# Kernel optimization log

Measured on AMD Instinct MI355X. Metric: run time of the kernel, lower is better.

The kernel has to match this reference:

```python
import jax, jax.numpy as jnp
import numpy as np

VOCAB = 67
EMB = 32
BRANCH = 32
OUT = 96
L = 16
B = 131072


def setup_inputs() -> dict:
    key = jax.random.key(0)
    ks = jax.random.split(key, 10)
    x = jax.random.randint(ks[0], (B, L), 0, VOCAB, dtype=jnp.int64)
    embed = jax.random.normal(ks[1], (VOCAB, EMB), dtype=jnp.float32) * 0.1
    w2 = jax.random.normal(ks[2], (BRANCH, EMB, 2), dtype=jnp.float32) * 0.1
    b2 = jnp.zeros((BRANCH,), jnp.float32)
    w3 = jax.random.normal(ks[3], (BRANCH, EMB, 3), dtype=jnp.float32) * 0.1
    b3 = jnp.zeros((BRANCH,), jnp.float32)
    w4 = jax.random.normal(ks[4], (BRANCH, EMB, 4), dtype=jnp.float32) * 0.1
    b4 = jnp.zeros((BRANCH,), jnp.float32)
    pw = jax.random.normal(ks[5], (OUT, 3 * BRANCH), dtype=jnp.float32) * 0.02
    pb = jnp.zeros((OUT,), jnp.float32)
    return {"x": x, "embed": embed, "w2": w2, "b2": b2, "w3": w3,
            "b3": b3, "w4": w4, "b4": b4, "pw": pw, "pb": pb}


def _branch(emb_ncl, w, b):
    # emb_ncl: [B, EMB, L]; w: [BRANCH, EMB, k] -> conv valid, ReLU, max over time
    y = jax.lax.conv_general_dilated(
        emb_ncl, w, window_strides=(1,), padding='VALID',
        dimension_numbers=('NCH', 'OIH', 'NCH'))
    y = jax.nn.relu(y + b[None, :, None])
    return jnp.max(y, axis=2)  # [B, BRANCH]


def reference(x, embed, w2, b2, w3, b3, w4, b4, pw, pb):
    # padding_idx=0: row 0 of the table is zeros
    table = embed.at[0].set(0.0)
    emb = table[x]                      # [B, L, EMB]
    emb = jnp.transpose(emb, (0, 2, 1))  # [B, EMB, L]
    g2 = _branch(emb, w2, b2)
    g3 = _branch(emb, w3, b3)
    g4 = _branch(emb, w4, b4)
    feat = jnp.concatenate([g2, g3, g4], axis=1)  # [B, 96]
    # Linear + ReLU (dropout is identity at eval)
    return jax.nn.relu(feat @ pw.T + pb)
```

## Files before the change

### kernel.cpp

```cpp
#include <hip/hip_runtime.h>
#include <hip/hip_fp16.h>


#define VOCABSZ 67
#define EMBSZ   32
#define NCH     32
#define NFEAT   96
#define SEQL    16
#define BATCH   131072
#define NTAB    9
#define NFP     (NFEAT / 2)
#define TABU    9648
#define PWOFF   9648
#define NPW     4608
#define CNTW    14336
#define NCHUNK  1024
#define ESTR    80
#define LTS     (VOCABSZ * ESTR)
#define LDSB    (NTAB * LTS + 16)

typedef _Float16 v2h __attribute__((ext_vector_type(2)));
typedef _Float16 v8h __attribute__((ext_vector_type(8)));
typedef float    v4f __attribute__((ext_vector_type(4)));

__device__ __forceinline__ unsigned packh2(float a, float b) {
    v2h p; p[0] = (_Float16)a; p[1] = (_Float16)b;
    return __builtin_bit_cast(unsigned, p);
}

__global__ __launch_bounds__(256) void build_tables(
    const float* __restrict__ embed,
    const float* __restrict__ w2, const float* __restrict__ b2,
    const float* __restrict__ w3, const float* __restrict__ b3,
    const float* __restrict__ w4, const float* __restrict__ b4,
    const float* __restrict__ pw,
    unsigned* __restrict__ ws)
{
    int idx = blockIdx.x * 256 + threadIdx.x;
    if (idx == CNTW) ws[idx] = 0u;
    if (idx < TABU) {
        int cp = idx & 15;
        int t  = idx >> 4;
        int j  = t / VOCABSZ;
        int v  = t - j * VOCABSZ;
        const float* w; const float* bias; int k, h;
        if (j < 2)      { w = w2; k = 2; h = j;     bias = (h == 0) ? b2 : nullptr; }
        else if (j < 5) { w = w3; k = 3; h = j - 2; bias = (h == 0) ? b3 : nullptr; }
        else            { w = w4; k = 4; h = j - 5; bias = (h == 0) ? b4 : nullptr; }
        int c0 = 2 * cp;
        float a0 = bias ? bias[c0]     : 0.0f;
        float a1 = bias ? bias[c0 + 1] : 0.0f;
        if (v != 0) {
            #pragma unroll
            for (int e = 0; e < EMBSZ; ++e) {
                float ev = embed[v * EMBSZ + e];
                a0 += ev * w[((c0    ) * EMBSZ + e) * k + h];
                a1 += ev * w[((c0 + 1) * EMBSZ + e) * k + h];
            }
        }
        ws[t * 16 + cp] = packh2(a0, a1);
    } else if (idx < TABU + NPW) {
        int i  = idx - PWOFF;
        int o  = i / NFP;
        int fp = i - o * NFP;
        ws[PWOFF + i] = packh2(pw[o * NFEAT + 2 * fp], pw[o * NFEAT + 2 * fp + 1]);
    }
}

template<int K, int N, int P0, int TB>
__device__ __forceinline__ void lconv(const char* __restrict__ base,
                                      const int (&ap)[16], v8h& m)
{
    v8h s[N];
    #pragma unroll
    for (int u = 0; u < N; ++u)
        s[u] = *reinterpret_cast<const v8h*>(base + TB + ap[P0 + u]);
    #pragma unroll
    for (int h = 1; h < K; ++h) {
        v8h t[N];
        #pragma unroll
        for (int u = 0; u < N; ++u)
            t[u] = *reinterpret_cast<const v8h*>(base + TB + h * LTS + ap[P0 + u + h]);
        #pragma unroll
        for (int u = 0; u < N; ++u) s[u] = s[u] + t[u];
    }
    #pragma unroll
    for (int u = 0; u < N; ++u) m = __builtin_elementwise_max(m, s[u]);
}

__global__ __launch_bounds__(512, 6) void fused_cnn(
    const int*      __restrict__ x,
    unsigned*       __restrict__ ws,
    const float*    __restrict__ pb,
    float*          __restrict__ out)
{
    extern __shared__ __align__(16) char ldsraw[];
    const int tid = threadIdx.x;
    {
        const float4* s4 = reinterpret_cast<const float4*>(ws);
        float4* d4 = reinterpret_cast<float4*>(ldsraw);
        #pragma unroll
        for (int i0 = 0; i0 < 2560; i0 += 512) {
            int i = i0 + tid;
            if (i < 2412) {
                int t = i >> 2, cc = i & 3;
                d4[5 * t + cc] = s4[i];
            }
        }
    }
    volatile int* slot = reinterpret_cast<volatile int*>(ldsraw + NTAB * LTS);
    unsigned* cnt = ws + CNTW;

    const int lane = tid & 63;
    const int wv   = tid >> 6;
    const int ml   = lane & 15;
    const int c    = lane >> 4;
    const int co   = c << 4;
    const char* base = ldsraw;
    const unsigned* __restrict__ pwp = ws + PWOFF + ml * NFP + c * 4;

    for (;;) {
        if (tid == 0) *slot = (int)atomicAdd(cnt, 1u);
        __syncthreads();
        const int chunk = *slot;
        __syncthreads();
        if (chunk >= NCHUNK) break;

        const int rowb = chunk * 128 + wv * 16;
        const int row  = rowb + ml;

        const int4* xp = reinterpret_cast<const int4*>(x + row * SEQL);
        int4 q0 = xp[0], q1 = xp[1], q2 = xp[2], q3 = xp[3];
        int ap[16];
        ap[ 0] = q0.x * ESTR + co; ap[ 1] = q0.y * ESTR + co;
        ap[ 2] = q0.z * ESTR + co; ap[ 3] = q0.w * ESTR + co;
        ap[ 4] = q1.x * ESTR + co; ap[ 5] = q1.y * ESTR + co;
        ap[ 6] = q1.z * ESTR + co; ap[ 7] = q1.w * ESTR + co;
        ap[ 8] = q2.x * ESTR + co; ap[ 9] = q2.y * ESTR + co;
        ap[10] = q2.z * ESTR + co; ap[11] = q2.w * ESTR + co;
        ap[12] = q3.x * ESTR + co; ap[13] = q3.y * ESTR + co;
        ap[14] = q3.z * ESTR + co; ap[15] = q3.w * ESTR + co;

        v8h m2 = {}, m3 = {}, m4 = {};
        lconv<2, 5,  0, 0 * LTS>(base, ap, m2);
        lconv<2, 5,  5, 0 * LTS>(base, ap, m2);
        lconv<2, 5, 10, 0 * LTS>(base, ap, m2);
        lconv<3, 5,  0, 2 * LTS>(base, ap, m3);
        lconv<3, 5,  5, 2 * LTS>(base, ap, m3);
        lconv<3, 4, 10, 2 * LTS>(base, ap, m3);
        lconv<4, 5,  0, 5 * LTS>(base, ap, m4);
        lconv<4, 4,  5, 5 * LTS>(base, ap, m4);
        lconv<4, 4,  9, 5 * LTS>(base, ap, m4);

        #pragma unroll
        for (int u = 0; u < 6; ++u) {
            v4f acc = {0.f, 0.f, 0.f, 0.f};
            v8h w0 = *reinterpret_cast<const v8h*>(pwp + 768 * u);
            v8h w1 = *reinterpret_cast<const v8h*>(pwp + 768 * u + 16);
            v8h w2 = *reinterpret_cast<const v8h*>(pwp + 768 * u + 32);
            acc = __builtin_amdgcn_mfma_f32_16x16x32_f16(m2, w0, acc, 0, 0, 0);
            acc = __builtin_amdgcn_mfma_f32_16x16x32_f16(m3, w1, acc, 0, 0, 0);
            acc = __builtin_amdgcn_mfma_f32_16x16x32_f16(m4, w2, acc, 0, 0, 0);
            float pbl = pb[16 * u + ml];
            #pragma unroll
            for (int r = 0; r < 4; ++r)
                out[(size_t)(rowb + c * 4 + r) * NFEAT + 16 * u + ml] =
                    fmaxf(acc[r] + pbl, 0.f);
        }
    }
}

extern "C" void kernel_launch(void* const* d_in, const int* in_sizes, int n_in,
                              void* d_out, int out_size, void* d_ws, size_t ws_size,
                              hipStream_t stream)
{
    const int*   x     = (const int*)  d_in[0];
    const float* embed = (const float*)d_in[1];
    const float* w2    = (const float*)d_in[2];
    const float* b2    = (const float*)d_in[3];
    const float* w3    = (const float*)d_in[4];
    const float* b3    = (const float*)d_in[5];
    const float* w4    = (const float*)d_in[6];
    const float* b4    = (const float*)d_in[7];
    const float* pw    = (const float*)d_in[8];
    const float* pb    = (const float*)d_in[9];
    float* out = (float*)d_out;
    unsigned* ws = (unsigned*)d_ws;

    build_tables<<<(CNTW + 256) / 256, 256, 0, stream>>>(
        embed, w2, b2, w3, b3, w4, b4, pw, ws);

    (void)hipFuncSetAttribute((const void*)fused_cnn,
                              hipFuncAttributeMaxDynamicSharedMemorySize,
                              LDSB);
    fused_cnn<<<768, 512, LDSB, stream>>>(x, ws, pb, out);
}
```

Before: 49.45 us.

## Replace persistent atomic-scheduled blocks with one-chunk-per-block grid and unpadded LDS tables

Drops the persistent-kernel loop that fetched 128-row chunks through a global atomic counter, and instead launches one block per chunk (1024 blocks), removing the atomic, the two barriers per chunk and the counter reset. The LDS table row stride shrinks from 80 to 64 bytes, so the table copy becomes a straight contiguous copy and addresses are computed with shifts. The smaller LDS footprint allows raising the launch-bounds occupancy hint from 6 to 8. The trade-off is that every block now reloads the full LDS table once per chunk rather than once per persistent block, and the unpadded stride may increase LDS bank conflicts.

```diff
diff --git a/kernel.cpp b/kernel.cpp
--- a/kernel.cpp
+++ b/kernel.cpp
@@ -13,11 +13,9 @@
 #define TABU    9648
 #define PWOFF   9648
 #define NPW     4608
-#define CNTW    14336
-#define NCHUNK  1024
-#define ESTR    80
+#define ESTR    64
 #define LTS     (VOCABSZ * ESTR)
-#define LDSB    (NTAB * LTS + 16)
+#define LDSB    (NTAB * LTS)
 
 typedef _Float16 v2h __attribute__((ext_vector_type(2)));
 typedef _Float16 v8h __attribute__((ext_vector_type(8)));
@@ -37,7 +35,6 @@
     unsigned* __restrict__ ws)
 {
     int idx = blockIdx.x * 256 + threadIdx.x;
-    if (idx == CNTW) ws[idx] = 0u;
     if (idx < TABU) {
         int cp = idx & 15;
         int t  = idx >> 4;
@@ -88,9 +85,9 @@
     for (int u = 0; u < N; ++u) m = __builtin_elementwise_max(m, s[u]);
 }
 
-__global__ __launch_bounds__(512, 6) void fused_cnn(
+__global__ __launch_bounds__(512, 8) void fused_cnn(
     const int*      __restrict__ x,
-    unsigned*       __restrict__ ws,
+    const unsigned* __restrict__ ws,
     const float*    __restrict__ pb,
     float*          __restrict__ out)
 {
@@ -102,71 +99,59 @@
         #pragma unroll
         for (int i0 = 0; i0 < 2560; i0 += 512) {
             int i = i0 + tid;
-            if (i < 2412) {
-                int t = i >> 2, cc = i & 3;
-                d4[5 * t + cc] = s4[i];
-            }
+            if (i < 2412) d4[i] = s4[i];
         }
     }
-    volatile int* slot = reinterpret_cast<volatile int*>(ldsraw + NTAB * LTS);
-    unsigned* cnt = ws + CNTW;
+    __syncthreads();
 
     const int lane = tid & 63;
     const int wv   = tid >> 6;
     const int ml   = lane & 15;
     const int c    = lane >> 4;
     const int co   = c << 4;
+    const int rowb = blockIdx.x * 128 + wv * 16;
+    const int row  = rowb + ml;
     const char* base = ldsraw;
+
+    const int4* xp = reinterpret_cast<const int4*>(x + row * SEQL);
+    int4 q0 = xp[0], q1 = xp[1], q2 = xp[2], q3 = xp[3];
+    int ap[16];
+    ap[ 0] = (q0.x << 6) + co; ap[ 1] = (q0.y << 6) + co;
+    ap[ 2] = (q0.z << 6) + co; ap[ 3] = (q0.w << 6) + co;
+    ap[ 4] = (q1.x << 6) + co; ap[ 5] = (q1.y << 6) + co;
+    ap[ 6] = (q1.z << 6) + co; ap[ 7] = (q1.w << 6) + co;
+    ap[ 8] = (q2.x << 6) + co; ap[ 9] = (q2.y << 6) + co;
+    ap[10] = (q2.z << 6) + co; ap[11] = (q2.w << 6) + co;
+    ap[12] = (q3.x << 6) + co; ap[13] = (q3.y << 6) + co;
+    ap[14] = (q3.z << 6) + co; ap[15] = (q3.w << 6) + co;
+
+    v8h m2 = {}, m3 = {}, m4 = {};
+
+    lconv<2, 5,  0, 0 * LTS>(base, ap, m2);
+    lconv<2, 5,  5, 0 * LTS>(base, ap, m2);
+    lconv<2, 5, 10, 0 * LTS>(base, ap, m2);
+    lconv<3, 5,  0, 2 * LTS>(base, ap, m3);
+    lconv<3, 5,  5, 2 * LTS>(base, ap, m3);
+    lconv<3, 4, 10, 2 * LTS>(base, ap, m3);
+    lconv<4, 5,  0, 5 * LTS>(base, ap, m4);
+    lconv<4, 4,  5, 5 * LTS>(base, ap, m4);
+    lconv<4, 4,  9, 5 * LTS>(base, ap, m4);
+
     const unsigned* __restrict__ pwp = ws + PWOFF + ml * NFP + c * 4;
-
-    for (;;) {
-        if (tid == 0) *slot = (int)atomicAdd(cnt, 1u);
-        __syncthreads();
-        const int chunk = *slot;
-        __syncthreads();
-        if (chunk >= NCHUNK) break;
-
-        const int rowb = chunk * 128 + wv * 16;
-        const int row  = rowb + ml;
-
-        const int4* xp = reinterpret_cast<const int4*>(x + row * SEQL);
-        int4 q0 = xp[0], q1 = xp[1], q2 = xp[2], q3 = xp[3];
-        int ap[16];
-        ap[ 0] = q0.x * ESTR + co; ap[ 1] = q0.y * ESTR + co;
-        ap[ 2] = q0.z * ESTR + co; ap[ 3] = q0.w * ESTR + co;
-        ap[ 4] = q1.x * ESTR + co; ap[ 5] = q1.y * ESTR + co;
-        ap[ 6] = q1.z * ESTR + co; ap[ 7] = q1.w * ESTR + co;
-        ap[ 8] = q2.x * ESTR + co; ap[ 9] = q2.y * ESTR + co;
-        ap[10] = q2.z * ESTR + co; ap[11] = q2.w * ESTR + co;
-        ap[12] = q3.x * ESTR + co; ap[13] = q3.y * ESTR + co;
-        ap[14] = q3.z * ESTR + co; ap[15] = q3.w * ESTR + co;
-
-        v8h m2 = {}, m3 = {}, m4 = {};
-        lconv<2, 5,  0, 0 * LTS>(base, ap, m2);
-        lconv<2, 5,  5, 0 * LTS>(base, ap, m2);
-        lconv<2, 5, 10, 0 * LTS>(base, ap, m2);
-        lconv<3, 5,  0, 2 * LTS>(base, ap, m3);
-        lconv<3, 5,  5, 2 * LTS>(base, ap, m3);
-        lconv<3, 4, 10, 2 * LTS>(base, ap, m3);
-        lconv<4, 5,  0, 5 * LTS>(base, ap, m4);
-        lconv<4, 4,  5, 5 * LTS>(base, ap, m4);
-        lconv<4, 4,  9, 5 * LTS>(base, ap, m4);
-
+    #pragma unroll
+    for (int u = 0; u < 6; ++u) {
+        v4f acc = {0.f, 0.f, 0.f, 0.f};
+        v8h w0 = *reinterpret_cast<const v8h*>(pwp + 768 * u);
+        v8h w1 = *reinterpret_cast<const v8h*>(pwp + 768 * u + 16);
+        v8h w2 = *reinterpret_cast<const v8h*>(pwp + 768 * u + 32);
+        acc = __builtin_amdgcn_mfma_f32_16x16x32_f16(m2, w0, acc, 0, 0, 0);
+        acc = __builtin_amdgcn_mfma_f32_16x16x32_f16(m3, w1, acc, 0, 0, 0);
+        acc = __builtin_amdgcn_mfma_f32_16x16x32_f16(m4, w2, acc, 0, 0, 0);
+        float pbl = pb[16 * u + ml];
         #pragma unroll
-        for (int u = 0; u < 6; ++u) {
-            v4f acc = {0.f, 0.f, 0.f, 0.f};
-            v8h w0 = *reinterpret_cast<const v8h*>(pwp + 768 * u);
-            v8h w1 = *reinterpret_cast<const v8h*>(pwp + 768 * u + 16);
-            v8h w2 = *reinterpret_cast<const v8h*>(pwp + 768 * u + 32);
-            acc = __builtin_amdgcn_mfma_f32_16x16x32_f16(m2, w0, acc, 0, 0, 0);
-            acc = __builtin_amdgcn_mfma_f32_16x16x32_f16(m3, w1, acc, 0, 0, 0);
-            acc = __builtin_amdgcn_mfma_f32_16x16x32_f16(m4, w2, acc, 0, 0, 0);
-            float pbl = pb[16 * u + ml];
-            #pragma unroll
-            for (int r = 0; r < 4; ++r)
-                out[(size_t)(rowb + c * 4 + r) * NFEAT + 16 * u + ml] =
-                    fmaxf(acc[r] + pbl, 0.f);
-        }
+        for (int r = 0; r < 4; ++r)
+            out[(size_t)(rowb + c * 4 + r) * NFEAT + 16 * u + ml] =
+                fmaxf(acc[r] + pbl, 0.f);
     }
 }
 
@@ -187,11 +172,8 @@
     float* out = (float*)d_out;
     unsigned* ws = (unsigned*)d_ws;
 
-    build_tables<<<(CNTW + 256) / 256, 256, 0, stream>>>(
+    build_tables<<<(TABU + NPW + 255) / 256, 256, 0, stream>>>(
         embed, w2, b2, w3, b3, w4, b4, pw, ws);
 
-    (void)hipFuncSetAttribute((const void*)fused_cnn,
-                              hipFuncAttributeMaxDynamicSharedMemorySize,
-                              LDSB);
-    fused_cnn<<<768, 512, LDSB, stream>>>(x, ws, pb, out);
+    fused_cnn<<<BATCH / 128, 512, LDSB, stream>>>(x, ws, pb, out);
 }
```

New measurement: 48.42 us. -2.1%, faster.
